# Optimization experiments

Hardware: AMD Instinct MI355X
Metric: run time of the kernel (lower is better)

Reference implementation:

```python
import jax, jax.numpy as jnp
import numpy as np

# direction id -> (lat_shift, lon_shift)
WIND_DIRS = [(0, 0), (-1, 0), (-1, 1), (0, 1), (1, 1), (1, 0), (1, -1), (0, -1), (-1, -1)]
SWIN_SHIFT = (1, 3, 6)       # (pl, lat, lon)
WIND_SHIFT_SCALE = 2
LAT_REGIONS, LON_REGIONS = 4, 8
NUM_DIRS = 9


def setup_inputs() -> dict:
    key = jax.random.key(0)
    k1, k2 = jax.random.split(key)
    x = jax.random.normal(k1, (2, 14, 128, 256, 96), dtype=jnp.float32)
    wind_direction_id = jax.random.randint(k2, (2, 128, 256), 0, NUM_DIRS)
    return {"x": x, "wind_direction_id": wind_direction_id}


def _regional_dominant_dirs(wid):
    # wid: (B, H, W) int -> (B, LAT_REGIONS, LON_REGIONS) dominant direction per region
    B, H, W = wid.shape
    r = wid.reshape(B, LAT_REGIONS, H // LAT_REGIONS, LON_REGIONS, W // LON_REGIONS)
    counts = jnp.sum(jax.nn.one_hot(r, NUM_DIRS, dtype=jnp.float32), axis=(2, 4))  # (B, latR, lonR, 9)
    return jnp.argmax(counts, axis=-1)  # ties -> first max, matching torch bincount().argmax()


def reference(x, wind_direction_id):
    # x: (B, Pl, Lat, Lon, C); wind_direction_id: (B, H, W) in [0, 9)
    B, Pl, Lat, Lon, C = x.shape
    # 1) Swin fixed shift (negative roll on Pl, Lat, Lon)
    sp, sl, so = SWIN_SHIFT
    x = jnp.roll(x, (-sp, -sl, -so), axis=(1, 2, 3))
    # 2) per-region dominant wind direction
    rd = _regional_dominant_dirs(wind_direction_id)  # (B, latR, lonR)
    # nearest-neighbor upsample to full grid (matches F.interpolate mode='nearest')
    ih = (jnp.arange(Lat) * LAT_REGIONS) // Lat
    iw = (jnp.arange(Lon) * LON_REGIONS) // Lon
    dirs_up = rd[:, ih][:, :, iw]  # (B, Lat, Lon)
    # 3) mask & combine over the 9 rolled versions
    combined = jnp.zeros_like(x)
    for dir_id, (lat_s, lon_s) in enumerate(WIND_DIRS):
        als, alo = lat_s * WIND_SHIFT_SCALE, lon_s * WIND_SHIFT_SCALE
        shifted = x if (als == 0 and alo == 0) else jnp.roll(x, (als, alo), axis=(2, 3))
        mask = (dirs_up == dir_id).astype(x.dtype)[:, None, :, :, None]  # (B,1,Lat,Lon,1)
        combined = combined + shifted * mask
    # 4) global dominant direction (returned as stat)
    counts = jnp.bincount(wind_direction_id.reshape(-1), length=NUM_DIRS)
    dominant_id = jnp.argmax(counts)
    return combined, dominant_id
```

## Files before the change

### kernel.cpp

```cpp
#include <hip/hip_runtime.h>

namespace {
constexpr int kB   = 2;
constexpr int kPl  = 14;
constexpr int kLat = 128;
constexpr int kLon = 256;
constexpr int kC   = 96;
constexpr int kNumDirs = 9;
constexpr int kC4  = kC / 4;
constexpr int kNTotal = kB * kPl * kLat * kLon * kC;
constexpr int kN4 = kNTotal / 4;
}

__device__ __constant__ int c_lat_s[kNumDirs] = {0,-1,-1, 0, 1, 1, 1, 0,-1};
__device__ __constant__ int c_lon_s[kNumDirs] = {0, 0, 1, 1, 1, 0,-1,-1,-1};

__global__ void zero_counts_kernel(int* __restrict__ gcounts) {
    if (threadIdx.x < kNumDirs) gcounts[threadIdx.x] = 0;
}

__global__ __launch_bounds__(256) void region_dirs_kernel(
        const int* __restrict__ wid, int* __restrict__ rdpack,
        int* __restrict__ gcounts) {
    __shared__ int cnt[kNumDirs];
    const int t = threadIdx.x;
    if (t < kNumDirs) cnt[t] = 0;
    __syncthreads();

    const int blk  = blockIdx.x;
    const int rlon = blk & 7;
    const int rlat = (blk >> 3) & 3;
    const int b    = blk >> 5;

    for (int k = t; k < 1024; k += 256) {
        const int i  = k >> 5;
        const int j  = k & 31;
        const int la = rlat * 32 + i;
        const int lo = rlon * 32 + j;
        const int d  = wid[(b * kLat + la) * kLon + lo];
        atomicAdd(&cnt[d], 1);
    }
    __syncthreads();

    if (t == 0) {
        int best = 0, bestc = cnt[0];
        #pragma unroll
        for (int d = 1; d < kNumDirs; ++d) {
            if (cnt[d] > bestc) { bestc = cnt[d]; best = d; }
        }
        const int dla = 3 - 2 * c_lat_s[best];
        const int dlo = 6 - 2 * c_lon_s[best];
        rdpack[blk] = (dla << 8) | dlo;
    }
    if (t < kNumDirs) atomicAdd(&gcounts[t], cnt[t]);
}

__global__ void finalize_kernel(const int* __restrict__ gcounts,
                                float* __restrict__ out_dom) {
    int best = 0, bestc = gcounts[0];
    #pragma unroll
    for (int d = 1; d < kNumDirs; ++d) {
        if (gcounts[d] > bestc) { bestc = gcounts[d]; best = d; }
    }
    *out_dom = (float)best;
}

__global__ __launch_bounds__(256) void gather_kernel(
        const float4* __restrict__ x, const int* __restrict__ rdpack,
        float4* __restrict__ out) {
    const int stride = gridDim.x * blockDim.x;
    for (int i = blockIdx.x * blockDim.x + threadIdx.x; i < kN4; i += stride) {
        const int c4 = i % kC4;
        int r = i / kC4;
        const int lo = r & (kLon - 1); r >>= 8;
        const int la = r & (kLat - 1); r >>= 7;
        const int p  = r % kPl;
        const int b  = r / kPl;

        const int pack = rdpack[(b * 4 + (la >> 5)) * 8 + (lo >> 5)];
        const int lasrc = (la + (pack >> 8)) & (kLat - 1);
        const int losrc = (lo + (pack & 0xff)) & (kLon - 1);
        int psrc = p + 1; if (psrc >= kPl) psrc = 0;

        const int src = (((b * kPl + psrc) * kLat + lasrc) * kLon + losrc) * kC4 + c4;
        out[i] = x[src];
    }
}

extern "C" void kernel_launch(void* const* d_in, const int* in_sizes, int n_in,
                              void* d_out, int out_size, void* d_ws, size_t ws_size,
                              hipStream_t stream) {
    const float* x   = (const float*)d_in[0];
    const int*   wid = (const int*)d_in[1];
    float* out = (float*)d_out;

    int* gcounts = (int*)d_ws;
    int* rdpack  = gcounts + 16;

    zero_counts_kernel<<<1, 64, 0, stream>>>(gcounts);
    region_dirs_kernel<<<kB * 4 * 8, 256, 0, stream>>>(wid, rdpack, gcounts);
    finalize_kernel<<<1, 1, 0, stream>>>(gcounts, out + kNTotal);

    const int blocks = 4096;
    gather_kernel<<<blocks, 256, 0, stream>>>((const float4*)x, rdpack,
                                              (float4*)out);
}
```

Baseline: 144.9 us.

## Fold global-count finalize into gather kernel and use nontemporal copies

```diff
diff --git a/kernel.cpp b/kernel.cpp
--- a/kernel.cpp
+++ b/kernel.cpp
@@ -10,18 +10,19 @@
 constexpr int kC4  = kC / 4;
 constexpr int kNTotal = kB * kPl * kLat * kLon * kC;
 constexpr int kN4 = kNTotal / 4;
+constexpr int kRegions = kB * 4 * 8;
+constexpr int kCopyBlocks = 1024;
+constexpr int kItersPerThread = kN4 / (kCopyBlocks * 256);
 }
+
+typedef float f4 __attribute__((ext_vector_type(4)));
 
 __device__ __constant__ int c_lat_s[kNumDirs] = {0,-1,-1, 0, 1, 1, 1, 0,-1};
 __device__ __constant__ int c_lon_s[kNumDirs] = {0, 0, 1, 1, 1, 0,-1,-1,-1};
 
-__global__ void zero_counts_kernel(int* __restrict__ gcounts) {
-    if (threadIdx.x < kNumDirs) gcounts[threadIdx.x] = 0;
-}
-
 __global__ __launch_bounds__(256) void region_dirs_kernel(
         const int* __restrict__ wid, int* __restrict__ rdpack,
-        int* __restrict__ gcounts) {
+        int* __restrict__ cnt_blk) {
     __shared__ int cnt[kNumDirs];
     const int t = threadIdx.x;
     if (t < kNumDirs) cnt[t] = 0;
@@ -37,39 +38,51 @@
         const int j  = k & 31;
         const int la = rlat * 32 + i;
         const int lo = rlon * 32 + j;
-        const int d  = wid[(b * kLat + la) * kLon + lo];
-        atomicAdd(&cnt[d], 1);
+        atomicAdd(&cnt[wid[(b * kLat + la) * kLon + lo]], 1);
     }
     __syncthreads();
 
+    if (t < kNumDirs) cnt_blk[blk * kNumDirs + t] = cnt[t];
     if (t == 0) {
         int best = 0, bestc = cnt[0];
         #pragma unroll
-        for (int d = 1; d < kNumDirs; ++d) {
+        for (int d = 1; d < kNumDirs; ++d)
             if (cnt[d] > bestc) { bestc = cnt[d]; best = d; }
-        }
         const int dla = 3 - 2 * c_lat_s[best];
         const int dlo = 6 - 2 * c_lon_s[best];
         rdpack[blk] = (dla << 8) | dlo;
     }
-    if (t < kNumDirs) atomicAdd(&gcounts[t], cnt[t]);
-}
-
-__global__ void finalize_kernel(const int* __restrict__ gcounts,
-                                float* __restrict__ out_dom) {
-    int best = 0, bestc = gcounts[0];
-    #pragma unroll
-    for (int d = 1; d < kNumDirs; ++d) {
-        if (gcounts[d] > bestc) { bestc = gcounts[d]; best = d; }
-    }
-    *out_dom = (float)best;
 }
 
 __global__ __launch_bounds__(256) void gather_kernel(
-        const float4* __restrict__ x, const int* __restrict__ rdpack,
-        float4* __restrict__ out) {
-    const int stride = gridDim.x * blockDim.x;
-    for (int i = blockIdx.x * blockDim.x + threadIdx.x; i < kN4; i += stride) {
+        const f4* __restrict__ x, const int* __restrict__ rdpack,
+        const int* __restrict__ cnt_blk, f4* __restrict__ out,
+        float* __restrict__ out_dom) {
+    if (blockIdx.x == kCopyBlocks) {
+        __shared__ int tot[kNumDirs];
+        const int t = threadIdx.x;
+        if (t < kNumDirs) {
+            int s = 0;
+            for (int r = 0; r < kRegions; ++r) s += cnt_blk[r * kNumDirs + t];
+            tot[t] = s;
+        }
+        __syncthreads();
+        if (t == 0) {
+            int best = 0, bestc = tot[0];
+            #pragma unroll
+            for (int d = 1; d < kNumDirs; ++d)
+                if (tot[d] > bestc) { bestc = tot[d]; best = d; }
+            *out_dom = (float)best;
+        }
+        return;
+    }
+
+    const int base = blockIdx.x * 256 + threadIdx.x;
+    constexpr int kStride = kCopyBlocks * 256;
+
+    #pragma unroll 4
+    for (int k = 0; k < kItersPerThread; ++k) {
+        const int i = base + k * kStride;
         const int c4 = i % kC4;
         int r = i / kC4;
         const int lo = r & (kLon - 1); r >>= 8;
@@ -83,7 +96,8 @@
         int psrc = p + 1; if (psrc >= kPl) psrc = 0;
 
         const int src = (((b * kPl + psrc) * kLat + lasrc) * kLon + losrc) * kC4 + c4;
-        out[i] = x[src];
+        const f4 v = __builtin_nontemporal_load(&x[src]);
+        __builtin_nontemporal_store(v, &out[i]);
     }
 }
 
@@ -94,14 +108,10 @@
     const int*   wid = (const int*)d_in[1];
     float* out = (float*)d_out;
 
-    int* gcounts = (int*)d_ws;
-    int* rdpack  = gcounts + 16;
+    int* rdpack  = (int*)d_ws;
+    int* cnt_blk = rdpack + kRegions;
 
-    zero_counts_kernel<<<1, 64, 0, stream>>>(gcounts);
-    region_dirs_kernel<<<kB * 4 * 8, 256, 0, stream>>>(wid, rdpack, gcounts);
-    finalize_kernel<<<1, 1, 0, stream>>>(gcounts, out + kNTotal);
-
-    const int blocks = 4096;
-    gather_kernel<<<blocks, 256, 0, stream>>>((const float4*)x, rdpack,
-                                              (float4*)out);
+    region_dirs_kernel<<<kRegions, 256, 0, stream>>>(wid, rdpack, cnt_blk);
+    gather_kernel<<<kCopyBlocks + 1, 256, 0, stream>>>(
+        (const f4*)x, rdpack, cnt_blk, (f4*)out, out + kNTotal);
 }
```

Result: faster. 140.9 us (-2.8%).
